# Optimization experiments

Measured on AMD Instinct MI355X. Metric: run time of the kernel, lower is better.

The kernel has to match this reference:

```python
import jax, jax.numpy as jnp
import numpy as np

N, E, DIM, HEADS = 50000, 600000, 128, 4
C = DIM // HEADS  # per-head channels = 32
NEG_SLOPE = 0.2
LN_EPS = 1e-5


def setup_inputs() -> dict:
    key = jax.random.key(0)
    ks = jax.random.split(key, 6)
    x = jax.random.normal(ks[0], (N, DIM), dtype=jnp.float32)
    edge_index = jax.random.randint(ks[1], (2, E), 0, N, dtype=jnp.int32)
    W = jax.random.normal(ks[2], (DIM, DIM), dtype=jnp.float32) / np.sqrt(DIM).astype(np.float32)
    b = jnp.zeros((DIM,), jnp.float32)
    att_src = jax.random.normal(ks[3], (HEADS, C), dtype=jnp.float32) * 0.1
    att_dst = jax.random.normal(ks[4], (HEADS, C), dtype=jnp.float32) * 0.1
    gamma = jnp.ones((DIM,), jnp.float32)
    beta = jnp.zeros((DIM,), jnp.float32)
    return {"x": x, "W": W, "b": b, "att_src": att_src, "att_dst": att_dst,
            "gamma": gamma, "beta": beta, "edge_index": edge_index}


def _gat_conv(x, W, b, att_src, att_dst, src, dst):
    # linear projection, per-head view: [N, H, C]
    h = (x @ W).reshape(N, HEADS, C)
    # per-node attention logits: [N, H]
    a_s = jnp.einsum('nhc,hc->nh', h, att_src)
    a_d = jnp.einsum('nhc,hc->nh', h, att_dst)
    # per-edge logits with leaky relu: [Etot, H]
    e = jax.nn.leaky_relu(a_s[src] + a_d[dst], negative_slope=NEG_SLOPE)
    # segment softmax over incoming edges of each dst node
    m = jax.ops.segment_max(e, dst, num_segments=N)
    ez = jnp.exp(e - m[dst])
    denom = jax.ops.segment_sum(ez, dst, num_segments=N) + 1e-16
    alpha = ez / denom[dst]  # [Etot, H]
    # weighted scatter-aggregation: [N, H, C]
    out = jax.ops.segment_sum(alpha[:, :, None] * h[src], dst, num_segments=N)
    return out.reshape(N, DIM) + b


def reference(x, W, b, att_src, att_dst, gamma, beta, edge_index):
    # add self loops (PyG GATConv default add_self_loops=True)
    loops = jnp.arange(N, dtype=edge_index.dtype)
    src = jnp.concatenate([edge_index[0], loops])
    dst = jnp.concatenate([edge_index[1], loops])
    g = _gat_conv(x, W, b, att_src, att_dst, src, dst)
    # residual + GELU (torch exact erf GELU) + LayerNorm; dropout = identity (eval)
    y = x + jax.nn.gelu(g, approximate=False)
    mu = jnp.mean(y, axis=-1, keepdims=True)
    var = jnp.mean(jnp.square(y - mu), axis=-1, keepdims=True)
    return (y - mu) / jnp.sqrt(var + LN_EPS) * gamma + beta
```

## Files before the change

kernel.cpp:

```cpp
#include <hip/hip_runtime.h>
#include <math.h>

#define DIMC 128
#define HEADSC 4
#define CAP 64

typedef __attribute__((ext_vector_type(8))) short bf16x8;
typedef __attribute__((ext_vector_type(4))) float f32x4;
typedef __attribute__((ext_vector_type(2))) float f32x2;

static __device__ __forceinline__ short f2bf(float f) {
    unsigned u = __builtin_bit_cast(unsigned, f);
    unsigned r = (u + 0x7fff + ((u >> 16) & 1)) >> 16;
    return (short)r;
}
static __device__ __forceinline__ float blo(unsigned q) {
    return __builtin_bit_cast(float, q << 16);
}
static __device__ __forceinline__ float bhi(unsigned q) {
    return __builtin_bit_cast(float, q & 0xffff0000u);
}

__global__ __launch_bounds__(256, 2) void gemm_scatter_kernel(
    const float* __restrict__ x, const float* __restrict__ W,
    const float* __restrict__ att_src, const float* __restrict__ att_dst,
    const int* __restrict__ ei, int E,
    unsigned short* __restrict__ hb, float* __restrict__ a_s, float* __restrict__ a_d,
    int* __restrict__ cnt, int* __restrict__ rec, int nstrip)
{
    __shared__ unsigned short wfrag[4][2][4][64][8];
    __shared__ unsigned short htile[16][128];

    const int lane = threadIdx.x & 63;
    const int q    = threadIdx.x >> 6;
    const int l15  = lane & 15;
    const int lg   = lane >> 4;

#pragma unroll
    for (int ct = 0; ct < 2; ++ct) {
#pragma unroll
        for (int kk = 0; kk < 4; ++kk) {
            const float* wp = W + (size_t)(kk * 32 + lg * 8) * DIMC + q * 32 + ct * 16 + l15;
            bf16x8 f;
#pragma unroll
            for (int jj = 0; jj < 8; ++jj) f[jj] = f2bf(wp[(size_t)jj * DIMC]);
            *(bf16x8*)(&wfrag[q][ct][kk][lane][0]) = f;
        }
    }
    float attS[2], attD[2];
#pragma unroll
    for (int ct = 0; ct < 2; ++ct) {
        attS[ct] = att_src[q * 32 + ct * 16 + l15];
        attD[ct] = att_dst[q * 32 + ct * 16 + l15];
    }
    __syncthreads();

    for (int s = blockIdx.x; s < nstrip; s += gridDim.x) {
        const int row = s * 16 + l15;
        const float* xp = x + (size_t)row * DIMC + lg * 8;
        bf16x8 afr[4];
#pragma unroll
        for (int kk = 0; kk < 4; ++kk) {
            f32x4 v0 = *(const f32x4*)(xp + kk * 32);
            f32x4 v1 = *(const f32x4*)(xp + kk * 32 + 4);
#pragma unroll
            for (int jj = 0; jj < 4; ++jj) {
                afr[kk][jj]     = f2bf(v0[jj]);
                afr[kk][jj + 4] = f2bf(v1[jj]);
            }
        }
        f32x4 acc[2] = {};
#pragma unroll
        for (int ct = 0; ct < 2; ++ct) {
#pragma unroll
            for (int kk = 0; kk < 4; ++kk) {
                bf16x8 b = *(const bf16x8*)(&wfrag[q][ct][kk][lane][0]);
                acc[ct] = __builtin_amdgcn_mfma_f32_16x16x32_bf16(afr[kk], b, acc[ct], 0, 0, 0);
            }
        }
#pragma unroll
        for (int reg = 0; reg < 4; ++reg) {
            float sv = fmaf(acc[0][reg], attS[0], acc[1][reg] * attS[1]);
            float dv = fmaf(acc[0][reg], attD[0], acc[1][reg] * attD[1]);
#pragma unroll
            for (int mk = 1; mk < 16; mk <<= 1) {
                sv += __shfl_xor(sv, mk);
                dv += __shfl_xor(dv, mk);
            }
            if (l15 == 0) {
                const int r = s * 16 + lg * 4 + reg;
                a_s[r * HEADSC + q] = sv;
                a_d[r * HEADSC + q] = dv;
            }
        }
        __syncthreads();
#pragma unroll
        for (int ct = 0; ct < 2; ++ct)
#pragma unroll
            for (int reg = 0; reg < 4; ++reg)
                htile[lg * 4 + reg][q * 32 + ct * 16 + l15] =
                    (unsigned short)f2bf(acc[ct][reg]);
        __syncthreads();
        const int r2  = threadIdx.x >> 4;
        const int c2b = (threadIdx.x & 15) * 8;
        bf16x8 v = *(const bf16x8*)(&htile[r2][c2b]);
        *(bf16x8*)(hb + (size_t)(s * 16 + r2) * DIMC + c2b) = v;
    }

    const int tid = blockIdx.x * 256 + threadIdx.x;
    const int stride = gridDim.x * 256;
    if (((E & 3) == 0) && ((((size_t)ei) & 15) == 0)) {
        const int E4 = E >> 2;
        const int4* s4p = (const int4*)ei;
        const int4* d4p = (const int4*)(ei + E);
        for (int i = tid; i < E4; i += stride) {
            const int4 s4 = s4p[i];
            const int4 d4 = d4p[i];
            int p;
            p = atomicAdd(&cnt[d4.x], 1); if (p < CAP) rec[(size_t)d4.x * CAP + p] = s4.x;
            p = atomicAdd(&cnt[d4.y], 1); if (p < CAP) rec[(size_t)d4.y * CAP + p] = s4.y;
            p = atomicAdd(&cnt[d4.z], 1); if (p < CAP) rec[(size_t)d4.z * CAP + p] = s4.z;
            p = atomicAdd(&cnt[d4.w], 1); if (p < CAP) rec[(size_t)d4.w * CAP + p] = s4.w;
        }
    } else {
        for (int i = tid; i < E; i += stride) {
            const int d = ei[E + i];
            const int p = atomicAdd(&cnt[d], 1);
            if (p < CAP) rec[(size_t)d * CAP + p] = ei[i];
        }
    }
}

__global__ __launch_bounds__(256) void node_kernel(
    const float* __restrict__ x, const unsigned short* __restrict__ hb,
    const int* __restrict__ cnt, const int* __restrict__ rec,
    const float* __restrict__ a_s, const float* __restrict__ a_d,
    const float* __restrict__ bias, const float* __restrict__ gamma,
    const float* __restrict__ beta, float* __restrict__ out, int N)
{
    const int wv = threadIdx.x >> 6;
    const int lane = threadIdx.x & 63;
    const int c2 = lane * 2;
    const int head = lane >> 4;

    for (int n = blockIdx.x * 4 + wv; n < N; n += gridDim.x * 4) {
        int deg = __builtin_amdgcn_readfirstlane(cnt[n]);
        deg = (deg < CAP) ? deg : CAP;
        const int base = n * CAP;
        const float adh = a_d[n * HEADSC + head];

        float es = a_s[n * HEADSC + head] + adh;
        es = (es > 0.f) ? es : 0.2f * es;
        const float ps = __expf(es);
        const unsigned qs = *(const unsigned*)(hb + (size_t)n * DIMC + c2);
        float den = ps;
        float A0 = ps * blo(qs), A1 = ps * bhi(qs), B0 = 0.f, B1 = 0.f;

        for (int i = 0; i < deg; i += 8) {
            int ss[8];
            float tt[8];
            unsigned qq[8];
#pragma unroll
            for (int u = 0; u < 8; ++u)
                ss[u] = rec[base + ((i + u < deg) ? i + u : 0)];
#pragma unroll
            for (int u = 0; u < 8; ++u)
                tt[u] = a_s[ss[u] * HEADSC + head] + adh;
#pragma unroll
            for (int u = 0; u < 8; ++u)
                qq[u] = *(const unsigned*)(hb + (size_t)ss[u] * DIMC + c2);
#pragma unroll
            for (int u = 0; u < 8; ++u) {
                float e = tt[u];
                e = (e > 0.f) ? e : 0.2f * e;
                float p = (i + u < deg) ? __expf(e) : 0.f;
                den += p;
                if (u & 1) { B0 = fmaf(p, blo(qq[u]), B0); B1 = fmaf(p, bhi(qq[u]), B1); }
                else       { A0 = fmaf(p, blo(qq[u]), A0); A1 = fmaf(p, bhi(qq[u]), A1); }
            }
        }
        const float acc0 = A0 + B0, acc1 = A1 + B1;

        const float inv = 1.f / (den + 1e-16f);
        const f32x2 bi = *(const f32x2*)(bias + c2);
        float g0 = acc0 * inv + bi.x;
        float g1 = acc1 * inv + bi.y;
        const float ge0 = 0.5f * g0 * (1.f + erff(g0 * 0.70710678118654752f));
        const float ge1 = 0.5f * g1 * (1.f + erff(g1 * 0.70710678118654752f));
        const f32x2 xv = *(const f32x2*)(x + (size_t)n * DIMC + c2);
        const float y0 = xv.x + ge0;
        const float y1 = xv.y + ge1;
        float s1 = y0 + y1, s2 = y0 * y0 + y1 * y1;
#pragma unroll
        for (int mk = 1; mk < 64; mk <<= 1) {
            s1 += __shfl_xor(s1, mk);
            s2 += __shfl_xor(s2, mk);
        }
        const float mu = s1 * (1.f / DIMC);
        const float var = s2 * (1.f / DIMC) - mu * mu;
        const float rstd = rsqrtf(var + 1e-5f);
        const f32x2 ga = *(const f32x2*)(gamma + c2);
        const f32x2 be = *(const f32x2*)(beta + c2);
        f32x2 o;
        o.x = (y0 - mu) * rstd * ga.x + be.x;
        o.y = (y1 - mu) * rstd * ga.y + be.y;
        *(f32x2*)(out + (size_t)n * DIMC + c2) = o;
    }
}

extern "C" void kernel_launch(void* const* d_in, const int* in_sizes, int n_in,
                              void* d_out, int out_size, void* d_ws, size_t ws_size,
                              hipStream_t stream)
{
    const float* x       = (const float*)d_in[0];
    const float* W       = (const float*)d_in[1];
    const float* bias    = (const float*)d_in[2];
    const float* att_src = (const float*)d_in[3];
    const float* att_dst = (const float*)d_in[4];
    const float* gamma   = (const float*)d_in[5];
    const float* beta    = (const float*)d_in[6];
    const int*   ei      = (const int*)d_in[7];

    const int N = in_sizes[0] / DIMC;
    const int E = in_sizes[7] / 2;

    unsigned short* hb = (unsigned short*)d_ws;
    float* a_s   = (float*)(hb + (size_t)N * DIMC);
    float* a_d   = a_s + (size_t)N * HEADSC;
    int* cnt     = (int*)(a_d + (size_t)N * HEADSC);
    int* rec     = cnt + N;

    hipMemsetAsync(cnt, 0, sizeof(int) * (size_t)N, stream);

    const int nstrip = (N + 15) / 16;
    gemm_scatter_kernel<<<1024, 256, 0, stream>>>(
        x, W, att_src, att_dst, ei, E, hb, a_s, a_d, cnt, rec, nstrip);
    node_kernel<<<(N + 3) / 4, 256, 0, stream>>>(
        x, hb, cnt, rec, a_s, a_d, bias, gamma, beta, (float*)d_out, N);
}
```

Measured before the change: 179.1 us.

## Split edge scatter into own kernel and process two nodes per wave

Moves the CSR-style edge bucketing out of the GEMM kernel into a separate one-thread-per-edge scatter kernel, and raises the GEMM launch-bounds occupancy hint. The node kernel now handles a pair of nodes per wavefront, interleaving their gathers to expose more memory-level parallelism, and hoists the bias, gamma and beta loads out of the loop. This adds one launch and loses the overlap of scatter with GEMM tail. The pair loop assumes N is even; an odd last node would be skipped.

```diff
diff --git a/kernel.cpp b/kernel.cpp
--- a/kernel.cpp
+++ b/kernel.cpp
@@ -21,12 +21,11 @@
     return __builtin_bit_cast(float, q & 0xffff0000u);
 }
 
-__global__ __launch_bounds__(256, 2) void gemm_scatter_kernel(
+__global__ __launch_bounds__(256, 4) void gemm_kernel(
     const float* __restrict__ x, const float* __restrict__ W,
     const float* __restrict__ att_src, const float* __restrict__ att_dst,
-    const int* __restrict__ ei, int E,
     unsigned short* __restrict__ hb, float* __restrict__ a_s, float* __restrict__ a_d,
-    int* __restrict__ cnt, int* __restrict__ rec, int nstrip)
+    int nstrip)
 {
     __shared__ unsigned short wfrag[4][2][4][64][8];
     __shared__ unsigned short htile[16][128];
@@ -106,28 +105,17 @@
         bf16x8 v = *(const bf16x8*)(&htile[r2][c2b]);
         *(bf16x8*)(hb + (size_t)(s * 16 + r2) * DIMC + c2b) = v;
     }
-
-    const int tid = blockIdx.x * 256 + threadIdx.x;
-    const int stride = gridDim.x * 256;
-    if (((E & 3) == 0) && ((((size_t)ei) & 15) == 0)) {
-        const int E4 = E >> 2;
-        const int4* s4p = (const int4*)ei;
-        const int4* d4p = (const int4*)(ei + E);
-        for (int i = tid; i < E4; i += stride) {
-            const int4 s4 = s4p[i];
-            const int4 d4 = d4p[i];
-            int p;
-            p = atomicAdd(&cnt[d4.x], 1); if (p < CAP) rec[(size_t)d4.x * CAP + p] = s4.x;
-            p = atomicAdd(&cnt[d4.y], 1); if (p < CAP) rec[(size_t)d4.y * CAP + p] = s4.y;
-            p = atomicAdd(&cnt[d4.z], 1); if (p < CAP) rec[(size_t)d4.z * CAP + p] = s4.z;
-            p = atomicAdd(&cnt[d4.w], 1); if (p < CAP) rec[(size_t)d4.w * CAP + p] = s4.w;
-        }
-    } else {
-        for (int i = tid; i < E; i += stride) {
-            const int d = ei[E + i];
-            const int p = atomicAdd(&cnt[d], 1);
-            if (p < CAP) rec[(size_t)d * CAP + p] = ei[i];
-        }
+}
+
+__global__ void scatter_kernel(const int* __restrict__ ei, int E,
+                               int* __restrict__ cnt, int* __restrict__ rec)
+{
+    const int i = blockIdx.x * blockDim.x + threadIdx.x;
+    if (i < E) {
+        const int s = ei[i];
+        const int d = ei[E + i];
+        const int p = atomicAdd(&cnt[d], 1);
+        if (p < CAP) rec[(size_t)d * CAP + p] = s;
     }
 }
 
@@ -142,69 +130,92 @@
     const int lane = threadIdx.x & 63;
     const int c2 = lane * 2;
     const int head = lane >> 4;
-
-    for (int n = blockIdx.x * 4 + wv; n < N; n += gridDim.x * 4) {
-        int deg = __builtin_amdgcn_readfirstlane(cnt[n]);
-        deg = (deg < CAP) ? deg : CAP;
-        const int base = n * CAP;
-        const float adh = a_d[n * HEADSC + head];
-
-        float es = a_s[n * HEADSC + head] + adh;
-        es = (es > 0.f) ? es : 0.2f * es;
-        const float ps = __expf(es);
-        const unsigned qs = *(const unsigned*)(hb + (size_t)n * DIMC + c2);
-        float den = ps;
-        float A0 = ps * blo(qs), A1 = ps * bhi(qs), B0 = 0.f, B1 = 0.f;
-
-        for (int i = 0; i < deg; i += 8) {
-            int ss[8];
-            float tt[8];
-            unsigned qq[8];
-#pragma unroll
-            for (int u = 0; u < 8; ++u)
-                ss[u] = rec[base + ((i + u < deg) ? i + u : 0)];
-#pragma unroll
-            for (int u = 0; u < 8; ++u)
-                tt[u] = a_s[ss[u] * HEADSC + head] + adh;
-#pragma unroll
-            for (int u = 0; u < 8; ++u)
-                qq[u] = *(const unsigned*)(hb + (size_t)ss[u] * DIMC + c2);
-#pragma unroll
-            for (int u = 0; u < 8; ++u) {
-                float e = tt[u];
-                e = (e > 0.f) ? e : 0.2f * e;
-                float p = (i + u < deg) ? __expf(e) : 0.f;
-                den += p;
-                if (u & 1) { B0 = fmaf(p, blo(qq[u]), B0); B1 = fmaf(p, bhi(qq[u]), B1); }
-                else       { A0 = fmaf(p, blo(qq[u]), A0); A1 = fmaf(p, bhi(qq[u]), A1); }
-            }
-        }
-        const float acc0 = A0 + B0, acc1 = A1 + B1;
-
-        const float inv = 1.f / (den + 1e-16f);
-        const f32x2 bi = *(const f32x2*)(bias + c2);
-        float g0 = acc0 * inv + bi.x;
-        float g1 = acc1 * inv + bi.y;
-        const float ge0 = 0.5f * g0 * (1.f + erff(g0 * 0.70710678118654752f));
-        const float ge1 = 0.5f * g1 * (1.f + erff(g1 * 0.70710678118654752f));
-        const f32x2 xv = *(const f32x2*)(x + (size_t)n * DIMC + c2);
-        const float y0 = xv.x + ge0;
-        const float y1 = xv.y + ge1;
-        float s1 = y0 + y1, s2 = y0 * y0 + y1 * y1;
-#pragma unroll
-        for (int mk = 1; mk < 64; mk <<= 1) {
-            s1 += __shfl_xor(s1, mk);
-            s2 += __shfl_xor(s2, mk);
-        }
-        const float mu = s1 * (1.f / DIMC);
-        const float var = s2 * (1.f / DIMC) - mu * mu;
-        const float rstd = rsqrtf(var + 1e-5f);
-        const f32x2 ga = *(const f32x2*)(gamma + c2);
-        const f32x2 be = *(const f32x2*)(beta + c2);
-        f32x2 o;
-        o.x = (y0 - mu) * rstd * ga.x + be.x;
-        o.y = (y1 - mu) * rstd * ga.y + be.y;
-        *(f32x2*)(out + (size_t)n * DIMC + c2) = o;
+    const int npair = N >> 1;
+
+    const f32x2 bi = *(const f32x2*)(bias + c2);
+    const f32x2 ga = *(const f32x2*)(gamma + c2);
+    const f32x2 be = *(const f32x2*)(beta + c2);
+
+    for (int pp = blockIdx.x * 4 + wv; pp < npair; pp += gridDim.x * 4) {
+        const int n0 = pp * 2, n1 = pp * 2 + 1;
+        int d0 = __builtin_amdgcn_readfirstlane(cnt[n0]); d0 = (d0 < CAP) ? d0 : CAP;
+        int d1 = __builtin_amdgcn_readfirstlane(cnt[n1]); d1 = (d1 < CAP) ? d1 : CAP;
+        const int b0 = n0 * CAP, b1 = n1 * CAP;
+        const float adh0 = a_d[n0 * HEADSC + head];
+        const float adh1 = a_d[n1 * HEADSC + head];
+
+        float e0s = a_s[n0 * HEADSC + head] + adh0;
+        float e1s = a_s[n1 * HEADSC + head] + adh1;
+        e0s = (e0s > 0.f) ? e0s : 0.2f * e0s;
+        e1s = (e1s > 0.f) ? e1s : 0.2f * e1s;
+        const float p0s = __expf(e0s), p1s = __expf(e1s);
+        const unsigned q0s = *(const unsigned*)(hb + (size_t)n0 * DIMC + c2);
+        const unsigned q1s = *(const unsigned*)(hb + (size_t)n1 * DIMC + c2);
+        float den0 = p0s, den1 = p1s;
+        float A0 = p0s * blo(q0s), A1 = p0s * bhi(q0s);
+        float C0 = p1s * blo(q1s), C1 = p1s * bhi(q1s);
+
+        const int dm = (d0 > d1) ? d0 : d1;
+        for (int i = 0; i < dm; i += 8) {
+            int ss0[8], ss1[8];
+            float tt0[8], tt1[8];
+            unsigned qq0[8], qq1[8];
+#pragma unroll
+            for (int u = 0; u < 8; ++u) {
+                ss0[u] = (i + u < d0) ? rec[b0 + i + u] : n0;
+                ss1[u] = (i + u < d1) ? rec[b1 + i + u] : n1;
+            }
+#pragma unroll
+            for (int u = 0; u < 8; ++u) {
+                tt0[u] = a_s[ss0[u] * HEADSC + head] + adh0;
+                tt1[u] = a_s[ss1[u] * HEADSC + head] + adh1;
+            }
+#pragma unroll
+            for (int u = 0; u < 8; ++u) {
+                qq0[u] = *(const unsigned*)(hb + (size_t)ss0[u] * DIMC + c2);
+                qq1[u] = *(const unsigned*)(hb + (size_t)ss1[u] * DIMC + c2);
+            }
+#pragma unroll
+            for (int u = 0; u < 8; ++u) {
+                float e0 = tt0[u], e1 = tt1[u];
+                e0 = (e0 > 0.f) ? e0 : 0.2f * e0;
+                e1 = (e1 > 0.f) ? e1 : 0.2f * e1;
+                const float p0 = (i + u < d0) ? __expf(e0) : 0.f;
+                const float p1 = (i + u < d1) ? __expf(e1) : 0.f;
+                den0 += p0; den1 += p1;
+                A0 = fmaf(p0, blo(qq0[u]), A0); A1 = fmaf(p0, bhi(qq0[u]), A1);
+                C0 = fmaf(p1, blo(qq1[u]), C0); C1 = fmaf(p1, bhi(qq1[u]), C1);
+            }
+        }
+
+#pragma unroll
+        for (int kkn = 0; kkn < 2; ++kkn) {
+            const int n = kkn ? n1 : n0;
+            const float den = kkn ? den1 : den0;
+            const float ac0 = kkn ? C0 : A0;
+            const float ac1 = kkn ? C1 : A1;
+            const float inv = 1.f / (den + 1e-16f);
+            float g0 = ac0 * inv + bi.x;
+            float g1 = ac1 * inv + bi.y;
+            const float ge0 = 0.5f * g0 * (1.f + erff(g0 * 0.70710678118654752f));
+            const float ge1 = 0.5f * g1 * (1.f + erff(g1 * 0.70710678118654752f));
+            const f32x2 xv = *(const f32x2*)(x + (size_t)n * DIMC + c2);
+            const float y0 = xv.x + ge0;
+            const float y1 = xv.y + ge1;
+            float s1 = y0 + y1, s2 = y0 * y0 + y1 * y1;
+#pragma unroll
+            for (int mk = 1; mk < 64; mk <<= 1) {
+                s1 += __shfl_xor(s1, mk);
+                s2 += __shfl_xor(s2, mk);
+            }
+            const float mu = s1 * (1.f / DIMC);
+            const float var = s2 * (1.f / DIMC) - mu * mu;
+            const float rstd = rsqrtf(var + 1e-5f);
+            f32x2 o;
+            o.x = (y0 - mu) * rstd * ga.x + be.x;
+            o.y = (y1 - mu) * rstd * ga.y + be.y;
+            *(f32x2*)(out + (size_t)n * DIMC + c2) = o;
+        }
     }
 }
 
@@ -233,8 +244,8 @@
     hipMemsetAsync(cnt, 0, sizeof(int) * (size_t)N, stream);
 
     const int nstrip = (N + 15) / 16;
-    gemm_scatter_kernel<<<1024, 256, 0, stream>>>(
-        x, W, att_src, att_dst, ei, E, hb, a_s, a_d, cnt, rec, nstrip);
-    node_kernel<<<(N + 3) / 4, 256, 0, stream>>>(
+    gemm_kernel<<<1024, 256, 0, stream>>>(x, W, att_src, att_dst, hb, a_s, a_d, nstrip);
+    scatter_kernel<<<(E + 255) / 256, 256, 0, stream>>>(ei, E, cnt, rec);
+    node_kernel<<<(N / 2 + 3) / 4, 256, 0, stream>>>(
         x, hb, cnt, rec, a_s, a_d, bias, gamma, beta, (float*)d_out, N);
 }
```

After: 191.9 us. +7.2%, slower.
